# Kernel tuning notes

Hardware: AMD Instinct MI355X
Metric: run time of the kernel (lower is better)

## Reference

```python
import jax, jax.numpy as jnp
import numpy as np

B, T, C, NH, L, V = 2, 1024, 768, 12, 4, 50304
HS = C // NH  # 64


def _norm(x):
    # torch: (x - x.mean(-1)) / x.std(-1) with unbiased std (ddof=1)
    mu = jnp.mean(x, axis=-1, keepdims=True)
    sd = jnp.std(x, axis=-1, ddof=1, keepdims=True)
    return (x - mu) / sd


def setup_inputs() -> dict:
    key = jax.random.key(0)
    ks = jax.random.split(key, 8)
    idx = jax.random.randint(ks[0], (B, T), 0, V)
    wte = jax.random.normal(ks[1], (V, C), jnp.float32) * 0.02
    wpe = jax.random.normal(ks[2], (1024, C), jnp.float32) * 0.02
    c_attn_w = jax.random.normal(ks[3], (L, 3 * C, C), jnp.float32) * 0.02
    c_proj_w = jax.random.normal(ks[4], (L, C, C), jnp.float32) * 0.02
    w_decay = jax.random.uniform(ks[5], (L, C), jnp.float32)          # decay in [0,1)
    eta = jax.random.uniform(ks[6], (L, C), jnp.float32) * 0.01       # small, like 1/block_size init
    lm_head_w = jax.random.normal(ks[7], (V, C), jnp.float32) * 0.02
    return dict(idx=idx, wte=wte, wpe=wpe, c_attn_w=c_attn_w, c_proj_w=c_proj_w,
                w_decay=w_decay, eta=eta, lm_head_w=lm_head_w)


def _rwkv7_block(x, Wqkv, Wproj, wd, et):
    Bx, Tx, Cx = x.shape
    qkv = (x @ Wqkv.T).reshape(Bx, Tx, 3, NH, HS)
    qkv = _norm(qkv)
    # [T, B, nh, hs] each
    q = jnp.transpose(qkv[:, :, 0], (1, 0, 2, 3))
    k = jnp.transpose(qkv[:, :, 1], (1, 0, 2, 3))
    v = jnp.transpose(qkv[:, :, 2], (1, 0, 2, 3))
    q = jax.lax.erf(q)
    k = jax.lax.erf(k)
    wv = wd.reshape(NH, HS)   # decay per (head, channel i)
    ev = et.reshape(NH, HS)
    a = -k
    b = k * ev
    k_ = k * ev
    v_ = v

    def step(state, inp):
        q_t, a_t, b_t, k_t, v_t = inp
        # state: [B, nh, hs(i), hs(k)]
        sab = jnp.einsum('bhik,bhk,bhj->bhij', state, a_t, b_t)
        state = state * wv[None, :, :, None] + sab + jnp.einsum('bhj,bhi->bhij', k_t, v_t)
        out = jnp.einsum('bhj,bhij->bhi', q_t, state)
        return state, out

    state0 = jnp.zeros((Bx, NH, HS, HS), x.dtype)
    _, vt = jax.lax.scan(step, state0, (q, a, b, k_, v_))  # vt: [T, B, nh, hs]
    y = jnp.transpose(vt, (1, 0, 2, 3)).reshape(Bx, Tx, Cx) @ Wproj.T
    return x + y


def reference(idx, wte, wpe, c_attn_w, c_proj_w, w_decay, eta, lm_head_w):
    t = idx.shape[1]
    x = wte[idx] + wpe[:t][None]
    for l in range(L):
        x = _rwkv7_block(x, c_attn_w[l], c_proj_w[l], w_decay[l], eta[l])
    x = _norm(x)
    # targets=None path: logits for last position only
    logits = x[:, -1:, :] @ lm_head_w.T  # [B, 1, V]
    return logits
```

## Files before the change

kernel.cpp:

```cpp
#include <hip/hip_runtime.h>
#include <hip/hip_bf16.h>
#include <cmath>

using bf16   = __bf16;
using bf16x8 = __attribute__((ext_vector_type(8))) __bf16;
using bf16x4 = __attribute__((ext_vector_type(4))) __bf16;
using f32x4  = __attribute__((ext_vector_type(4))) float;
using u32x4  = __attribute__((ext_vector_type(4))) unsigned int;

__global__ __launch_bounds__(256) void cast4_kernel(const float* __restrict__ src,
                                                    bf16* __restrict__ dst, int n4) {
  int i = blockIdx.x * 256 + threadIdx.x;
  int stride = gridDim.x * 256;
  for (; i < n4; i += stride) {
    f32x4 v = ((const f32x4*)src)[i];
    bf16x4 o;
    o[0] = (bf16)v[0]; o[1] = (bf16)v[1]; o[2] = (bf16)v[2]; o[3] = (bf16)v[3];
    ((bf16x4*)dst)[i] = o;
  }
}

__global__ __launch_bounds__(256) void emb_kernel(const int* __restrict__ idx,
                                                  const float* __restrict__ wte,
                                                  const float* __restrict__ wpe,
                                                  float* __restrict__ xf,
                                                  bf16* __restrict__ xb) {
  int bt = blockIdx.x;
  int t = bt & 1023;
  int tok = idx[bt];
  const float* wr = wte + (long)tok * 768;
  const float* pr = wpe + (long)t * 768;
  for (int c = threadIdx.x; c < 768; c += 256) {
    float v = wr[c] + pr[c];
    xf[(long)bt * 768 + c] = v;
    xb[(long)bt * 768 + c] = (bf16)v;
  }
}

template <int PROJ>
__global__ __launch_bounds__(256) void gemm_kernel(const bf16* __restrict__ A,
                                                   const bf16* __restrict__ W,
                                                   float* __restrict__ out,
                                                   float* __restrict__ xf,
                                                   bf16* __restrict__ xb,
                                                   int N, int K) {
  __shared__ char ldsA[128 * 128];
  __shared__ char ldsB[128 * 128];
  const int tid = threadIdx.x;
  const int l = tid & 63, wid = tid >> 6;
  const int lr = l & 15, g = l >> 4;
  const int m0 = blockIdx.y * 128, n0 = blockIdx.x * 128;
  const int wm = wid >> 1, wn = wid & 1;

  f32x4 acc[4][4];
#pragma unroll
  for (int i = 0; i < 4; ++i)
#pragma unroll
    for (int j = 0; j < 4; ++j) acc[i][j] = {0.f, 0.f, 0.f, 0.f};

  for (int k0 = 0; k0 < K; k0 += 32) {
    __syncthreads();
#pragma unroll
    for (int it = 0; it < 2; ++it) {
      int slot = tid + it * 256;
      int row = slot >> 2, q = slot & 3;
      u32x4 da = *(const u32x4*)(A + (long)(m0 + row) * K + k0 + q * 8);
      *(u32x4*)(ldsA + row * 128 + ((q * 16) ^ ((row & 7) << 4))) = da;
      u32x4 db = *(const u32x4*)(W + (long)(n0 + row) * K + k0 + q * 8);
      *(u32x4*)(ldsB + row * 128 + ((q * 16) ^ ((row & 7) << 4))) = db;
    }
    __syncthreads();
    bf16x8 af[4], bfr[4];
#pragma unroll
    for (int it = 0; it < 4; ++it) {
      int row = wm * 64 + it * 16 + lr;
      af[it] = *(const bf16x8*)(ldsA + row * 128 + ((16 * g) ^ ((row & 7) << 4)));
    }
#pragma unroll
    for (int jt = 0; jt < 4; ++jt) {
      int row = wn * 64 + jt * 16 + lr;
      bfr[jt] = *(const bf16x8*)(ldsB + row * 128 + ((16 * g) ^ ((row & 7) << 4)));
    }
#pragma unroll
    for (int it = 0; it < 4; ++it)
#pragma unroll
      for (int jt = 0; jt < 4; ++jt)
        acc[it][jt] = __builtin_amdgcn_mfma_f32_16x16x32_bf16(af[it], bfr[jt], acc[it][jt], 0, 0, 0);
  }

#pragma unroll
  for (int it = 0; it < 4; ++it) {
#pragma unroll
    for (int jt = 0; jt < 4; ++jt) {
      int col = n0 + wn * 64 + jt * 16 + lr;
#pragma unroll
      for (int r = 0; r < 4; ++r) {
        int row = m0 + wm * 64 + it * 16 + g * 4 + r;
        if constexpr (PROJ) {
          long o = (long)row * 768 + col;
          float v = acc[it][jt][r] + xf[o];
          xf[o] = v;
          xb[o] = (bf16)v;
        } else {
          out[(long)row * N + col] = acc[it][jt][r];
        }
      }
    }
  }
}

__global__ __launch_bounds__(256) void normgram_kernel(const float* __restrict__ qkv,
                                                       const float* __restrict__ eta_l,
                                                       bf16* __restrict__ qG,
                                                       bf16* __restrict__ aG,
                                                       float* __restrict__ vG,
                                                       float* __restrict__ GaG,
                                                       bf16* __restrict__ GqG,
                                                       bf16* __restrict__ bTG) {
  const int bh = blockIdx.x >> 6, ch = blockIdx.x & 63;
  const int b = bh / 12, h = bh - b * 12;
  const int tid = threadIdx.x;
  __shared__ float raw[48][68];
  __shared__ float as[16][68], bs[16][68], qs[16][68];

  const long qbase = ((long)(b * 1024 + ch * 16)) * 2304 + h * 64;
#pragma unroll
  for (int i = 0; i < 3; ++i) {
    int slot = tid + i * 256;
    int c4 = slot & 15, sgrp = slot >> 4;
    int t = sgrp / 3, s = sgrp - 3 * t;
    f32x4 d = *(const f32x4*)(qkv + qbase + (long)t * 2304 + s * 768 + c4 * 4);
    *(f32x4*)(&raw[sgrp][c4 * 4]) = d;
  }
  __syncthreads();

  const int l = tid & 63, w = tid >> 6;
  const float ev = eta_l[h * 64 + l];
#pragma unroll
  for (int j = 0; j < 12; ++j) {
    int sgrp = w * 12 + j;
    int t = sgrp / 3, s = sgrp - 3 * t;
    float x = raw[sgrp][l];
    float mu = x;
#pragma unroll
    for (int o = 32; o; o >>= 1) mu += __shfl_xor(mu, o);
    mu *= (1.f / 64.f);
    float d = x - mu;
    float v2 = d * d;
#pragma unroll
    for (int o = 32; o; o >>= 1) v2 += __shfl_xor(v2, o);
    float sd = sqrtf(v2 * (1.f / 63.f));
    float gn = d / sd;
    long base = ((long)bh * 1024 + ch * 16 + t) * 64 + l;
    if (s == 0) {
      float qv = erff(gn);
      qs[t][l] = qv;
      qG[base] = (bf16)qv;
    } else if (s == 1) {
      float kh = erff(gn);
      as[t][l] = -kh;
      bs[t][l] = kh * ev;
      aG[base] = (bf16)(-kh);
    } else {
      vG[base] = gn;
    }
  }
  __syncthreads();

  const int t = tid & 15, u = tid >> 4;
  float dba = 0.f, dbq = 0.f;
#pragma unroll 4
  for (int d = 0; d < 64; ++d) {
    float bv = bs[u][d];
    dba += bv * as[t][d];
    dbq += bv * qs[t][d];
  }
  long g2 = (long)bh * 64 + ch;
  GaG[g2 * 256 + u * 16 + t] = (u < t) ? dba : 0.f;
  GqG[g2 * 512 + t * 32 + u] = (u <= t) ? (bf16)dbq : (bf16)0.f;
  GqG[g2 * 512 + t * 32 + 16 + u] = (bf16)0.f;
  int jj = tid >> 2, uq = tid & 3;
  bf16x8 pkv;
#pragma unroll
  for (int uu = 0; uu < 8; ++uu) pkv[uu] = (uq < 2) ? (bf16)bs[uq * 8 + uu][jj] : (bf16)0.f;
  *(bf16x8*)(bTG + g2 * 2048 + jj * 32 + uq * 8) = pkv;
}

__global__ __launch_bounds__(256) void scan_kernel(const float* __restrict__ wdl,
                                                   const bf16* __restrict__ aG,
                                                   const bf16* __restrict__ qG,
                                                   const float* __restrict__ vG,
                                                   const float* __restrict__ GaG,
                                                   const bf16* __restrict__ GqG,
                                                   const bf16* __restrict__ bTG,
                                                   bf16* __restrict__ yG) {
  const int bh = blockIdx.x;
  const int b = bh / 12, h = bh - b * 12;
  const int tid = threadIdx.x;
  const int l = tid & 63, wid = tid >> 6;
  const int lr = l & 15, g = l >> 4;

  __shared__ char sA[2][2][16 * 128];
  __shared__ char sQ[2][2][16 * 128];
  __shared__ char sB[2][2][64 * 64];
  __shared__ char sG[2][2][16 * 64];
  __shared__ float sGa[2][2][16][16];
  __shared__ float sV[2][2][16][64];
  __shared__ char sS[64 * 128];
  __shared__ float sM[16][68];

  const float* wrow = wdl + h * 64;
  const int irow = wid * 16 + lr;
  const float w_rec = fmaxf(wrow[irow], 0.004f);
  const float winv_rec = 1.0f / w_rec;

  float wc[4], w15c[4], l2wc[4];
#pragma unroll
  for (int r = 0; r < 4; ++r) {
    int row = wid * 16 + g * 4 + r;
    float w = fmaxf(wrow[row], 0.004f);
    wc[r] = w;
    l2wc[r] = log2f(w);
    w15c[r] = exp2f(15.0f * l2wc[r]);
  }

  f32x4 Sf[4];
#pragma unroll
  for (int j = 0; j < 4; ++j) Sf[j] = {0.f, 0.f, 0.f, 0.f};

  const long hTD = (long)bh * 1024 * 64;

  u32x4 rAQ[2], rB[2], rGG[2];
  f32x4 rV[2];

  auto LOAD2 = [&](int c0) {
#pragma unroll
    for (int k = 0; k < 2; ++k) {
      const int c = c0 + k;
      const long tb = hTD + (long)c * 16 * 64;
      const long g2 = (long)bh * 64 + c;
      if (tid < 128) {
        rAQ[k] = *(const u32x4*)(aG + tb + (tid >> 3) * 64 + (tid & 7) * 8);
      } else {
        rAQ[k] = *(const u32x4*)(qG + tb + ((tid - 128) >> 3) * 64 + ((tid - 128) & 7) * 8);
      }
      rB[k] = *(const u32x4*)(bTG + g2 * 2048 + (tid >> 2) * 32 + (tid & 3) * 8);
      if (tid < 64) {
        rGG[k] = *(const u32x4*)(GqG + g2 * 512 + (tid >> 2) * 32 + (tid & 3) * 8);
      } else if (tid < 128) {
        rGG[k] = *(const u32x4*)(GaG + g2 * 256 + ((tid - 64) >> 2) * 16 + ((tid - 64) & 3) * 4);
      }
      rV[k] = *(const f32x4*)(vG + tb + (tid >> 4) * 64 + (tid & 15) * 4);
    }
  };

  auto STORE2 = [&](int nb) {
#pragma unroll
    for (int k = 0; k < 2; ++k) {
      if (tid < 128) {
        int t = tid >> 3, q = tid & 7;
        *(u32x4*)(sA[nb][k] + t * 128 + ((q * 16) ^ ((t & 7) << 4))) = rAQ[k];
      } else {
        int t = (tid - 128) >> 3, q = (tid - 128) & 7;
        *(u32x4*)(sQ[nb][k] + t * 128 + ((q * 16) ^ ((t & 7) << 4))) = rAQ[k];
      }
      {
        int j = tid >> 2, q = tid & 3;
        *(u32x4*)(sB[nb][k] + j * 64 + ((q * 16) ^ ((j & 3) << 4))) = rB[k];
      }
      if (tid < 64) {
        int t = tid >> 2, q = tid & 3;
        *(u32x4*)(sG[nb][k] + t * 64 + ((q * 16) ^ ((t & 3) << 4))) = rGG[k];
      } else if (tid < 128) {
        int u = (tid - 64) >> 2, q = (tid - 64) & 3;
        *(u32x4*)(&sGa[nb][k][u][q * 4]) = rGG[k];
      }
      {
        int t = tid >> 4, i4 = tid & 15;
        *(f32x4*)(&sV[nb][k][t][i4 * 4]) = rV[k];
      }
    }
  };

  auto COMPUTE = [&](int cur, int cip, int ch) {
    const char* pA = sA[cur][cip];
    const char* pQ = sQ[cur][cip];
    const char* pB = sB[cur][cip];
    const char* pG = sG[cur][cip];
    const float* pGa = &sGa[cur][cip][0][0];
    const float* pV = &sV[cur][cip][0][0] + irow;
    const float* pM = &sM[0][0] + irow;

    asm volatile("s_waitcnt lgkmcnt(0)" ::: "memory");
    __builtin_amdgcn_sched_barrier(0);

    f32x4 mf = {0.f, 0.f, 0.f, 0.f}, mqf = {0.f, 0.f, 0.f, 0.f};
#pragma unroll
    for (int s = 0; s < 2; ++s) {
      bf16x8 af = *(const bf16x8*)(sS + irow * 128 + ((64 * s + 16 * g) ^ ((irow & 7) << 4)));
      bf16x8 ba = *(const bf16x8*)(pA + lr * 128 + ((64 * s + 16 * g) ^ ((lr & 7) << 4)));
      bf16x8 bq = *(const bf16x8*)(pQ + lr * 128 + ((64 * s + 16 * g) ^ ((lr & 7) << 4)));
      mf = __builtin_amdgcn_mfma_f32_16x16x32_bf16(af, ba, mf, 0, 0, 0);
      mqf = __builtin_amdgcn_mfma_f32_16x16x32_bf16(af, bq, mqf, 0, 0, 0);
    }
#pragma unroll
    for (int r = 0; r < 4; ++r) sM[lr][wid * 16 + g * 4 + r] = mf[r];
    asm volatile("s_waitcnt lgkmcnt(0)" ::: "memory");
    __builtin_amdgcn_sched_barrier(0);

    f32x4 acc4[4];
#pragma unroll
    for (int t = 0; t < 4; ++t) acc4[t] = {0.f, 0.f, 0.f, 0.f};
    bf16x8 zfrag;
#pragma unroll
    for (int i = 0; i < 8; ++i) zfrag[i] = (bf16)0.0f;
    float wp = 1.f, wpm1 = 0.f, wiv = 1.f;
#pragma unroll
    for (int u = 0; u < 16; ++u) {
      float muv = pM[u * 68];
      float vu = pV[u * 64];
      float c = wp * muv + wpm1 * acc4[u >> 2][u & 3];
      float zt = wiv * (c + vu);
      zfrag[u & 7] = (g == (u >> 3)) ? (bf16)zt : zfrag[u & 7];
      f32x4 ztv = {zt, zt, zt, zt};
#pragma unroll
      for (int q = 0; q < 4; ++q) {
        f32x4 ga = *(const f32x4*)(pGa + u * 16 + q * 4);
        acc4[q] = __builtin_elementwise_fma(ga, ztv, acc4[q]);
      }
      wpm1 = wp;
      wp *= w_rec;
      wiv *= winv_rec;
    }

#pragma unroll
    for (int jt = 0; jt < 4; ++jt) {
      int jrow = jt * 16 + lr;
      bf16x8 bb = *(const bf16x8*)(pB + jrow * 64 + ((16 * g) ^ ((jrow & 3) << 4)));
      f32x4 cs;
#pragma unroll
      for (int r = 0; r < 4; ++r) cs[r] = Sf[jt][r] * wc[r];
      f32x4 ns = __builtin_amdgcn_mfma_f32_16x16x32_bf16(zfrag, bb, cs, 0, 0, 0);
#pragma unroll
      for (int r = 0; r < 4; ++r) Sf[jt][r] = ns[r] * w15c[r];
    }

#pragma unroll
    for (int jt = 0; jt < 4; ++jt) {
#pragma unroll
      for (int r = 0; r < 4; ++r) {
        int row = wid * 16 + g * 4 + r;
        int d = jt * 16 + lr;
        *(bf16*)(sS + row * 128 + ((d * 2) ^ ((row & 7) << 4))) = (bf16)Sf[jt][r];
      }
    }

    {
      bf16x8 gq = *(const bf16x8*)(pG + lr * 64 + ((16 * g) ^ ((lr & 3) << 4)));
      f32x4 cy;
#pragma unroll
      for (int r = 0; r < 4; ++r) cy[r] = mqf[r] * wc[r];
      f32x4 yp = __builtin_amdgcn_mfma_f32_16x16x32_bf16(zfrag, gq, cy, 0, 0, 0);
      bf16x4 yo;
#pragma unroll
      for (int r = 0; r < 4; ++r) yo[r] = (bf16)(yp[r] * exp2f((float)lr * l2wc[r]));
      long yoff = ((long)b * 1024 + ch * 16 + lr) * 768 + h * 64 + wid * 16 + g * 4;
      *(bf16x4*)(yG + yoff) = yo;
    }
  };

  LOAD2(0);
  STORE2(0);
#pragma unroll
  for (int jt = 0; jt < 4; ++jt) {
#pragma unroll
    for (int r = 0; r < 4; ++r) {
      int row = wid * 16 + g * 4 + r;
      int d = jt * 16 + lr;
      *(bf16*)(sS + row * 128 + ((d * 2) ^ ((row & 7) << 4))) = (bf16)0.0f;
    }
  }
  __syncthreads();

  for (int gp = 0; gp < 32; ++gp) {
    const int cur = gp & 1;
    if (gp < 31) LOAD2(2 * gp + 2);
    COMPUTE(cur, 0, 2 * gp);
    COMPUTE(cur, 1, 2 * gp + 1);
    if (gp < 31) STORE2(cur ^ 1);
    __syncthreads();
  }
}

__global__ __launch_bounds__(256) void finalnorm_kernel(const float* __restrict__ xf,
                                                        float* __restrict__ xn) {
  __shared__ float red[4];
  int tid = threadIdx.x;
  for (int b = 0; b < 2; ++b) {
    const float* xr = xf + ((long)b * 1024 + 1023) * 768;
    float s = 0.f;
    for (int c = tid; c < 768; c += 256) s += xr[c];
#pragma unroll
    for (int o = 32; o; o >>= 1) s += __shfl_xor(s, o);
    if ((tid & 63) == 0) red[tid >> 6] = s;
    __syncthreads();
    float mu = (red[0] + red[1] + red[2] + red[3]) * (1.f / 768.f);
    __syncthreads();
    float s2 = 0.f;
    for (int c = tid; c < 768; c += 256) {
      float d = xr[c] - mu;
      s2 += d * d;
    }
#pragma unroll
    for (int o = 32; o; o >>= 1) s2 += __shfl_xor(s2, o);
    if ((tid & 63) == 0) red[tid >> 6] = s2;
    __syncthreads();
    float sd = sqrtf((red[0] + red[1] + red[2] + red[3]) * (1.f / 767.f));
    for (int c = tid; c < 768; c += 256) xn[b * 768 + c] = (xr[c] - mu) / sd;
    __syncthreads();
  }
}

__global__ __launch_bounds__(256) void lmhead_kernel(const float* __restrict__ W,
                                                     const float* __restrict__ xn,
                                                     float* __restrict__ out) {
  int l = threadIdx.x & 63, wid = threadIdx.x >> 6;
  int v0 = blockIdx.x * 64 + wid * 16;
  f32x4 x0[3], x1[3];
#pragma unroll
  for (int i = 0; i < 3; ++i) {
    x0[i] = *(const f32x4*)(xn + l * 4 + i * 256);
    x1[i] = *(const f32x4*)(xn + 768 + l * 4 + i * 256);
  }
  for (int vi = 0; vi < 16; ++vi) {
    const float* wr = W + (long)(v0 + vi) * 768;
    float pa = 0.f, pb = 0.f;
#pragma unroll
    for (int i = 0; i < 3; ++i) {
      f32x4 wv = *(const f32x4*)(wr + l * 4 + i * 256);
#pragma unroll
      for (int r = 0; r < 4; ++r) {
        pa += wv[r] * x0[i][r];
        pb += wv[r] * x1[i][r];
      }
    }
#pragma unroll
    for (int o = 32; o; o >>= 1) {
      pa += __shfl_xor(pa, o);
      pb += __shfl_xor(pb, o);
    }
    if (l == 0) {
      out[v0 + vi] = pa;
      out[50304 + v0 + vi] = pb;
    }
  }
}

extern "C" void kernel_launch(void* const* d_in, const int* in_sizes, int n_in,
                              void* d_out, int out_size, void* d_ws, size_t ws_size,
                              hipStream_t stream) {
  (void)in_sizes; (void)n_in; (void)out_size; (void)ws_size;
  const int*   idx      = (const int*)d_in[0];
  const float* wte      = (const float*)d_in[1];
  const float* wpe      = (const float*)d_in[2];
  const float* c_attn_w = (const float*)d_in[3];
  const float* c_proj_w = (const float*)d_in[4];
  const float* w_decay  = (const float*)d_in[5];
  const float* eta      = (const float*)d_in[6];
  const float* lm_head  = (const float*)d_in[7];
  float* out = (float*)d_out;

  char* ws = (char*)d_ws;
  size_t off = 0;
  auto alloc = [&](size_t bytes) -> char* {
    char* p = ws + off;
    off = (off + bytes + 255) & ~(size_t)255;
    return p;
  };
  float* xf   = (float*)alloc(2L * 1024 * 768 * 4);
  bf16*  xb   = (bf16*)alloc(2L * 1024 * 768 * 2);
  float* qkv  = (float*)alloc(2L * 1024 * 2304 * 4);
  bf16*  qGp  = (bf16*)alloc(24L * 1024 * 64 * 2);
  bf16*  aGp  = (bf16*)alloc(24L * 1024 * 64 * 2);
  float* vGp  = (float*)alloc(24L * 1024 * 64 * 4);
  float* GaGp = (float*)alloc(24L * 64 * 256 * 4);
  bf16*  GqGp = (bf16*)alloc(24L * 64 * 512 * 2);
  bf16*  bTGp = (bf16*)alloc(24L * 64 * 2048 * 2);
  bf16*  yGp  = (bf16*)alloc(2L * 1024 * 768 * 2);
  bf16*  WqB  = (bf16*)alloc(4L * 2304 * 768 * 2);
  bf16*  WpB  = (bf16*)alloc(4L * 768 * 768 * 2);
  float* xn   = (float*)alloc(2L * 768 * 4);

  cast4_kernel<<<dim3(2048), dim3(256), 0, stream>>>(c_attn_w, WqB, 4 * 2304 * 768 / 4);
  cast4_kernel<<<dim3(1024), dim3(256), 0, stream>>>(c_proj_w, WpB, 4 * 768 * 768 / 4);
  emb_kernel<<<dim3(2048), dim3(256), 0, stream>>>(idx, wte, wpe, xf, xb);

  for (int l = 0; l < 4; ++l) {
    gemm_kernel<0><<<dim3(18, 16), dim3(256), 0, stream>>>(
        xb, WqB + (long)l * 2304 * 768, qkv, nullptr, nullptr, 2304, 768);
    normgram_kernel<<<dim3(1536), dim3(256), 0, stream>>>(
        qkv, eta + l * 768, qGp, aGp, vGp, GaGp, GqGp, bTGp);
    scan_kernel<<<dim3(24), dim3(256), 0, stream>>>(
        w_decay + l * 768, aGp, qGp, vGp, GaGp, GqGp, bTGp, yGp);
    gemm_kernel<1><<<dim3(6, 16), dim3(256), 0, stream>>>(
        yGp, WpB + (long)l * 768 * 768, nullptr, xf, xb, 768, 768);
  }

  finalnorm_kernel<<<dim3(1), dim3(256), 0, stream>>>(xf, xn);
  lmhead_kernel<<<dim3(786), dim3(256), 0, stream>>>(lm_head, xn, out);
}
```

Baseline: 797.9 us.

## Split scan per head into four single-wave blocks over state row slices

The scan kernel now launches 96 single-wavefront blocks instead of 24 four-wave blocks. Each block owns 16 of the 64 state rows of one (batch, head) and processes one chunk per iteration. Because the rows of the state recurrence are independent, no cross-wave barrier is needed, so __syncthreads is dropped and the block relies on wave-local LDS ordering. The aim is to spread the serial scan across more CUs and remove block-level sync, at the cost of each block redundantly loading the shared A/Q/B/G chunk data.

```diff
diff --git a/kernel.cpp b/kernel.cpp
--- a/kernel.cpp
+++ b/kernel.cpp
@@ -151,18 +151,18 @@
     for (int o = 32; o; o >>= 1) v2 += __shfl_xor(v2, o);
     float sd = sqrtf(v2 * (1.f / 63.f));
     float gn = d / sd;
-    long base = ((long)bh * 1024 + ch * 16 + t) * 64 + l;
+    long rowb = ((long)bh * 1024 + ch * 16 + t) * 64;
     if (s == 0) {
       float qv = erff(gn);
       qs[t][l] = qv;
-      qG[base] = (bf16)qv;
+      qG[rowb + l] = (bf16)qv;
     } else if (s == 1) {
       float kh = erff(gn);
       as[t][l] = -kh;
       bs[t][l] = kh * ev;
-      aG[base] = (bf16)(-kh);
+      aG[rowb + l] = (bf16)(-kh);
     } else {
-      vG[base] = gn;
+      vG[rowb + l] = gn;
     }
   }
   __syncthreads();
@@ -186,39 +186,38 @@
   *(bf16x8*)(bTG + g2 * 2048 + jj * 32 + uq * 8) = pkv;
 }
 
-__global__ __launch_bounds__(256) void scan_kernel(const float* __restrict__ wdl,
-                                                   const bf16* __restrict__ aG,
-                                                   const bf16* __restrict__ qG,
-                                                   const float* __restrict__ vG,
-                                                   const float* __restrict__ GaG,
-                                                   const bf16* __restrict__ GqG,
-                                                   const bf16* __restrict__ bTG,
-                                                   bf16* __restrict__ yG) {
-  const int bh = blockIdx.x;
+__global__ __launch_bounds__(64) void scan_kernel(const float* __restrict__ wdl,
+                                                  const bf16* __restrict__ aG,
+                                                  const bf16* __restrict__ qG,
+                                                  const float* __restrict__ vG,
+                                                  const float* __restrict__ GaG,
+                                                  const bf16* __restrict__ GqG,
+                                                  const bf16* __restrict__ bTG,
+                                                  bf16* __restrict__ yG) {
+  const int bid = blockIdx.x;
+  const int bh = bid % 24, qi = bid / 24;
   const int b = bh / 12, h = bh - b * 12;
-  const int tid = threadIdx.x;
-  const int l = tid & 63, wid = tid >> 6;
-  const int lr = l & 15, g = l >> 4;
-
-  __shared__ char sA[2][2][16 * 128];
-  __shared__ char sQ[2][2][16 * 128];
-  __shared__ char sB[2][2][64 * 64];
-  __shared__ char sG[2][2][16 * 64];
-  __shared__ float sGa[2][2][16][16];
-  __shared__ float sV[2][2][16][64];
-  __shared__ char sS[64 * 128];
-  __shared__ float sM[16][68];
+  const int i0 = qi * 16;
+  const int l = threadIdx.x;
+  const int g = l >> 4, lr = l & 15;
+
+  __shared__ char  sA[2][16 * 128];
+  __shared__ char  sQ[2][16 * 128];
+  __shared__ char  sB[2][64 * 64];
+  __shared__ char  sG[2][16 * 64];
+  __shared__ float sGa[2][16][16];
+  __shared__ float sV[2][16][16];
+  __shared__ char  sS[16 * 128];
+  __shared__ float sM[16][17];
 
   const float* wrow = wdl + h * 64;
-  const int irow = wid * 16 + lr;
-  const float w_rec = fmaxf(wrow[irow], 0.004f);
-  const float winv_rec = 1.0f / w_rec;
+  const float w_rec = fmaxf(wrow[i0 + lr], 0.004f);
+  const float winv = 1.0f / w_rec;
 
   float wc[4], w15c[4], l2wc[4];
 #pragma unroll
   for (int r = 0; r < 4; ++r) {
-    int row = wid * 16 + g * 4 + r;
-    float w = fmaxf(wrow[row], 0.004f);
+    float w = fmaxf(wrow[i0 + g * 4 + r], 0.004f);
     wc[r] = w;
     l2wc[r] = log2f(w);
     w15c[r] = exp2f(15.0f * l2wc[r]);
@@ -228,83 +227,74 @@
 #pragma unroll
   for (int j = 0; j < 4; ++j) Sf[j] = {0.f, 0.f, 0.f, 0.f};
 
-  const long hTD = (long)bh * 1024 * 64;
-
-  u32x4 rAQ[2], rB[2], rGG[2];
-  f32x4 rV[2];
-
-  auto LOAD2 = [&](int c0) {
-#pragma unroll
-    for (int k = 0; k < 2; ++k) {
-      const int c = c0 + k;
-      const long tb = hTD + (long)c * 16 * 64;
-      const long g2 = (long)bh * 64 + c;
-      if (tid < 128) {
-        rAQ[k] = *(const u32x4*)(aG + tb + (tid >> 3) * 64 + (tid & 7) * 8);
-      } else {
-        rAQ[k] = *(const u32x4*)(qG + tb + ((tid - 128) >> 3) * 64 + ((tid - 128) & 7) * 8);
-      }
-      rB[k] = *(const u32x4*)(bTG + g2 * 2048 + (tid >> 2) * 32 + (tid & 3) * 8);
-      if (tid < 64) {
-        rGG[k] = *(const u32x4*)(GqG + g2 * 512 + (tid >> 2) * 32 + (tid & 3) * 8);
-      } else if (tid < 128) {
-        rGG[k] = *(const u32x4*)(GaG + g2 * 256 + ((tid - 64) >> 2) * 16 + ((tid - 64) & 3) * 4);
-      }
-      rV[k] = *(const f32x4*)(vG + tb + (tid >> 4) * 64 + (tid & 15) * 4);
-    }
+  const long hTD = (long)bh * 65536;
+  const long gB = (long)bh * 64;
+  const int tr = l >> 2, tq = l & 3;
+
+  u32x4 rA0, rA1, rQ0, rQ1, rB[4], rGq;
+  f32x4 rGa, rV;
+
+  auto LOAD = [&](int c) {
+    const long tb = hTD + (long)c * 1024;
+    const bf16* ap = aG + tb + tr * 64 + tq * 16;
+    rA0 = *(const u32x4*)(ap);
+    rA1 = *(const u32x4*)(ap + 8);
+    const bf16* qp = qG + tb + tr * 64 + tq * 16;
+    rQ0 = *(const u32x4*)(qp);
+    rQ1 = *(const u32x4*)(qp + 8);
+    const bf16* bp = bTG + (gB + c) * 2048 + l * 32;
+#pragma unroll
+    for (int k = 0; k < 4; ++k) rB[k] = *(const u32x4*)(bp + k * 8);
+    rGq = *(const u32x4*)(GqG + (gB + c) * 512 + tr * 32 + tq * 8);
+    rGa = *(const f32x4*)(GaG + (gB + c) * 256 + l * 4);
+    rV = *(const f32x4*)(vG + tb + tr * 64 + i0 + tq * 4);
   };
 
-  auto STORE2 = [&](int nb) {
-#pragma unroll
-    for (int k = 0; k < 2; ++k) {
-      if (tid < 128) {
-        int t = tid >> 3, q = tid & 7;
-        *(u32x4*)(sA[nb][k] + t * 128 + ((q * 16) ^ ((t & 7) << 4))) = rAQ[k];
-      } else {
-        int t = (tid - 128) >> 3, q = (tid - 128) & 7;
-        *(u32x4*)(sQ[nb][k] + t * 128 + ((q * 16) ^ ((t & 7) << 4))) = rAQ[k];
-      }
-      {
-        int j = tid >> 2, q = tid & 3;
-        *(u32x4*)(sB[nb][k] + j * 64 + ((q * 16) ^ ((j & 3) << 4))) = rB[k];
-      }
-      if (tid < 64) {
-        int t = tid >> 2, q = tid & 3;
-        *(u32x4*)(sG[nb][k] + t * 64 + ((q * 16) ^ ((t & 3) << 4))) = rGG[k];
-      } else if (tid < 128) {
-        int u = (tid - 64) >> 2, q = (tid - 64) & 3;
-        *(u32x4*)(&sGa[nb][k][u][q * 4]) = rGG[k];
-      }
-      {
-        int t = tid >> 4, i4 = tid & 15;
-        *(f32x4*)(&sV[nb][k][t][i4 * 4]) = rV[k];
-      }
-    }
+  auto STORE = [&](int nb) {
+    const int swzr = (tr & 7) << 4;
+    *(u32x4*)(sA[nb] + tr * 128 + ((tq * 32) ^ swzr)) = rA0;
+    *(u32x4*)(sA[nb] + tr * 128 + ((tq * 32 + 16) ^ swzr)) = rA1;
+    *(u32x4*)(sQ[nb] + tr * 128 + ((tq * 32) ^ swzr)) = rQ0;
+    *(u32x4*)(sQ[nb] + tr * 128 + ((tq * 32 + 16) ^ swzr)) = rQ1;
+#pragma unroll
+    for (int k = 0; k < 4; ++k)
+      *(u32x4*)(sB[nb] + l * 64 + ((k * 16) ^ ((l & 3) << 4))) = rB[k];
+    *(u32x4*)(sG[nb] + tr * 64 + ((tq * 16) ^ ((tr & 3) << 4))) = rGq;
+    *(f32x4*)(&sGa[nb][tr][tq * 4]) = rGa;
+    *(f32x4*)(&sV[nb][tr][tq * 4]) = rV;
   };
 
-  auto COMPUTE = [&](int cur, int cip, int ch) {
-    const char* pA = sA[cur][cip];
-    const char* pQ = sQ[cur][cip];
-    const char* pB = sB[cur][cip];
-    const char* pG = sG[cur][cip];
-    const float* pGa = &sGa[cur][cip][0][0];
-    const float* pV = &sV[cur][cip][0][0] + irow;
-    const float* pM = &sM[0][0] + irow;
-
+  LOAD(0);
+  STORE(0);
+#pragma unroll
+  for (int jt = 0; jt < 4; ++jt) {
+#pragma unroll
+    for (int r = 0; r < 4; ++r) {
+      int row = g * 4 + r;
+      int d = jt * 16 + lr;
+      *(bf16*)(sS + row * 128 + ((d * 2) ^ ((row & 7) << 4))) = (bf16)0.0f;
+    }
+  }
+
+  int cur = 0;
+  for (int c = 0; c < 64; ++c) {
     asm volatile("s_waitcnt lgkmcnt(0)" ::: "memory");
     __builtin_amdgcn_sched_barrier(0);
 
+    if (c < 63) LOAD(c + 1);
+
+    const int swz7 = (lr & 7) << 4, swz3 = (lr & 3) << 4;
     f32x4 mf = {0.f, 0.f, 0.f, 0.f}, mqf = {0.f, 0.f, 0.f, 0.f};
 #pragma unroll
     for (int s = 0; s < 2; ++s) {
-      bf16x8 af = *(const bf16x8*)(sS + irow * 128 + ((64 * s + 16 * g) ^ ((irow & 7) << 4)));
-      bf16x8 ba = *(const bf16x8*)(pA + lr * 128 + ((64 * s + 16 * g) ^ ((lr & 7) << 4)));
-      bf16x8 bq = *(const bf16x8*)(pQ + lr * 128 + ((64 * s + 16 * g) ^ ((lr & 7) << 4)));
+      bf16x8 af = *(const bf16x8*)(sS + lr * 128 + ((64 * s + 16 * g) ^ swz7));
+      bf16x8 ba = *(const bf16x8*)(sA[cur] + lr * 128 + ((64 * s + 16 * g) ^ swz7));
+      bf16x8 bq = *(const bf16x8*)(sQ[cur] + lr * 128 + ((64 * s + 16 * g) ^ swz7));
       mf = __builtin_amdgcn_mfma_f32_16x16x32_bf16(af, ba, mf, 0, 0, 0);
       mqf = __builtin_amdgcn_mfma_f32_16x16x32_bf16(af, bq, mqf, 0, 0, 0);
     }
 #pragma unroll
-    for (int r = 0; r < 4; ++r) sM[lr][wid * 16 + g * 4 + r] = mf[r];
+    for (int r = 0; r < 4; ++r) sM[lr][g * 4 + r] = mf[r];
     asm volatile("s_waitcnt lgkmcnt(0)" ::: "memory");
     __builtin_amdgcn_sched_barrier(0);
 
@@ -317,26 +307,28 @@
     float wp = 1.f, wpm1 = 0.f, wiv = 1.f;
 #pragma unroll
     for (int u = 0; u < 16; ++u) {
-      float muv = pM[u * 68];
-      float vu = pV[u * 64];
-      float c = wp * muv + wpm1 * acc4[u >> 2][u & 3];
-      float zt = wiv * (c + vu);
+      float muv = sM[u][lr];
+      float vu = sV[cur][u][lr];
+      float cc = wp * muv + wpm1 * acc4[u >> 2][u & 3];
+      float zt = wiv * (cc + vu);
       zfrag[u & 7] = (g == (u >> 3)) ? (bf16)zt : zfrag[u & 7];
       f32x4 ztv = {zt, zt, zt, zt};
 #pragma unroll
-      for (int q = 0; q < 4; ++q) {
-        f32x4 ga = *(const f32x4*)(pGa + u * 16 + q * 4);
-        acc4[q] = __builtin_elementwise_fma(ga, ztv, acc4[q]);
+      for (int qq = 0; qq < 4; ++qq) {
+        f32x4 ga = *(const f32x4*)(&sGa[cur][u][qq * 4]);
+        acc4[qq] = __builtin_elementwise_fma(ga, ztv, acc4[qq]);
       }
       wpm1 = wp;
       wp *= w_rec;
-      wiv *= winv_rec;
-    }
+      wiv *= winv;
+    }
+
+    if (c < 63) STORE(cur ^ 1);
 
 #pragma unroll
     for (int jt = 0; jt < 4; ++jt) {
       int jrow = jt * 16 + lr;
-      bf16x8 bb = *(const bf16x8*)(pB + jrow * 64 + ((16 * g) ^ ((jrow & 3) << 4)));
+      bf16x8 bb = *(const bf16x8*)(sB[cur] + jrow * 64 + ((16 * g) ^ ((jrow & 3) << 4)));
       f32x4 cs;
 #pragma unroll
       for (int r = 0; r < 4; ++r) cs[r] = Sf[jt][r] * wc[r];
@@ -349,14 +341,14 @@
     for (int jt = 0; jt < 4; ++jt) {
 #pragma unroll
       for (int r = 0; r < 4; ++r) {
-        int row = wid * 16 + g * 4 + r;
+        int row = g * 4 + r;
         int d = jt * 16 + lr;
         *(bf16*)(sS + row * 128 + ((d * 2) ^ ((row & 7) << 4))) = (bf16)Sf[jt][r];
       }
     }
 
     {
-      bf16x8 gq = *(const bf16x8*)(pG + lr * 64 + ((16 * g) ^ ((lr & 3) << 4)));
+      bf16x8 gq = *(const bf16x8*)(sG[cur] + lr * 64 + ((16 * g) ^ swz3));
       f32x4 cy;
 #pragma unroll
       for (int r = 0; r < 4; ++r) cy[r] = mqf[r] * wc[r];
@@ -364,31 +356,11 @@
       bf16x4 yo;
 #pragma unroll
       for (int r = 0; r < 4; ++r) yo[r] = (bf16)(yp[r] * exp2f((float)lr * l2wc[r]));
-      long yoff = ((long)b * 1024 + ch * 16 + lr) * 768 + h * 64 + wid * 16 + g * 4;
+      long yoff = ((long)b * 1024 + c * 16 + lr) * 768 + h * 64 + i0 + g * 4;
       *(bf16x4*)(yG + yoff) = yo;
     }
-  };
-
-  LOAD2(0);
-  STORE2(0);
-#pragma unroll
-  for (int jt = 0; jt < 4; ++jt) {
-#pragma unroll
-    for (int r = 0; r < 4; ++r) {
-      int row = wid * 16 + g * 4 + r;
-      int d = jt * 16 + lr;
-      *(bf16*)(sS + row * 128 + ((d * 2) ^ ((row & 7) << 4))) = (bf16)0.0f;
-    }
-  }
-  __syncthreads();
-
-  for (int gp = 0; gp < 32; ++gp) {
-    const int cur = gp & 1;
-    if (gp < 31) LOAD2(2 * gp + 2);
-    COMPUTE(cur, 0, 2 * gp);
-    COMPUTE(cur, 1, 2 * gp + 1);
-    if (gp < 31) STORE2(cur ^ 1);
-    __syncthreads();
+
+    cur ^= 1;
   }
 }
 
@@ -500,7 +472,7 @@
         xb, WqB + (long)l * 2304 * 768, qkv, nullptr, nullptr, 2304, 768);
     normgram_kernel<<<dim3(1536), dim3(256), 0, stream>>>(
         qkv, eta + l * 768, qGp, aGp, vGp, GaGp, GqGp, bTGp);
-    scan_kernel<<<dim3(24), dim3(256), 0, stream>>>(
+    scan_kernel<<<dim3(96), dim3(64), 0, stream>>>(
         w_decay + l * 768, aGp, qGp, vGp, GaGp, GqGp, bTGp, yGp);
     gemm_kernel<1><<<dim3(6, 16), dim3(256), 0, stream>>>(
         yGp, WpB + (long)l * 768 * 768, nullptr, xf, xb, 768, 768);
```

After: 921.0 us. +15.4%, slower.

## Fuse head norm and erf into QKV GEMM epilogue, merge prologue and final-norm kernels

Applied to the files above, without the earlier changes.

The QKV GEMM epilogue now does the per-head normalization, erf and eta scaling directly from the accumulators. It uses 16-lane shuffles across each 64-column head tile, which removes the fp32 qkv round trip through global memory. The former normgram kernel becomes a gram kernel that reads the bf16 q/a/b tensors. The weight casts and embedding are merged into one prologue launch, and the final norm is recomputed inside every lm_head block instead of running as a separate single-block kernel. In exchange, every lm_head block redundantly recomputes the norm, and the gram inputs are now rounded to bf16 where they used to be fp32.

```diff
diff --git a/kernel.cpp b/kernel.cpp
--- a/kernel.cpp
+++ b/kernel.cpp
@@ -8,42 +8,50 @@
 using f32x4  = __attribute__((ext_vector_type(4))) float;
 using u32x4  = __attribute__((ext_vector_type(4))) unsigned int;
 
-__global__ __launch_bounds__(256) void cast4_kernel(const float* __restrict__ src,
-                                                    bf16* __restrict__ dst, int n4) {
-  int i = blockIdx.x * 256 + threadIdx.x;
-  int stride = gridDim.x * 256;
-  for (; i < n4; i += stride) {
-    f32x4 v = ((const f32x4*)src)[i];
+__global__ __launch_bounds__(256) void prologue_kernel(const int* __restrict__ idx,
+                                                       const float* __restrict__ wte,
+                                                       const float* __restrict__ wpe,
+                                                       const float* __restrict__ c_attn_w,
+                                                       const float* __restrict__ c_proj_w,
+                                                       float* __restrict__ xf,
+                                                       bf16* __restrict__ xb,
+                                                       bf16* __restrict__ WqB,
+                                                       bf16* __restrict__ WpB) {
+  const int bid = blockIdx.x, tid = threadIdx.x;
+  if (bid < 2048) {
+    int t = bid & 1023;
+    int tok = idx[bid];
+    const float* wr = wte + (long)tok * 768;
+    const float* pr = wpe + (long)t * 768;
+    for (int c = tid; c < 768; c += 256) {
+      float v = wr[c] + pr[c];
+      xf[(long)bid * 768 + c] = v;
+      xb[(long)bid * 768 + c] = (bf16)v;
+    }
+  }
+  const int n4a = 4 * 2304 * 768 / 4;
+  for (int i = bid * 256 + tid; i < n4a; i += 4096 * 256) {
+    f32x4 v = ((const f32x4*)c_attn_w)[i];
     bf16x4 o;
     o[0] = (bf16)v[0]; o[1] = (bf16)v[1]; o[2] = (bf16)v[2]; o[3] = (bf16)v[3];
-    ((bf16x4*)dst)[i] = o;
-  }
-}
-
-__global__ __launch_bounds__(256) void emb_kernel(const int* __restrict__ idx,
-                                                  const float* __restrict__ wte,
-                                                  const float* __restrict__ wpe,
-                                                  float* __restrict__ xf,
-                                                  bf16* __restrict__ xb) {
-  int bt = blockIdx.x;
-  int t = bt & 1023;
-  int tok = idx[bt];
-  const float* wr = wte + (long)tok * 768;
-  const float* pr = wpe + (long)t * 768;
-  for (int c = threadIdx.x; c < 768; c += 256) {
-    float v = wr[c] + pr[c];
-    xf[(long)bt * 768 + c] = v;
-    xb[(long)bt * 768 + c] = (bf16)v;
-  }
-}
-
-template <int PROJ>
-__global__ __launch_bounds__(256) void gemm_kernel(const bf16* __restrict__ A,
-                                                   const bf16* __restrict__ W,
-                                                   float* __restrict__ out,
-                                                   float* __restrict__ xf,
-                                                   bf16* __restrict__ xb,
-                                                   int N, int K) {
+    ((bf16x4*)WqB)[i] = o;
+  }
+  const int n4p = 4 * 768 * 768 / 4;
+  for (int i = bid * 256 + tid; i < n4p; i += 4096 * 256) {
+    f32x4 v = ((const f32x4*)c_proj_w)[i];
+    bf16x4 o;
+    o[0] = (bf16)v[0]; o[1] = (bf16)v[1]; o[2] = (bf16)v[2]; o[3] = (bf16)v[3];
+    ((bf16x4*)WpB)[i] = o;
+  }
+}
+
+__global__ __launch_bounds__(256) void gemmqkv_kernel(const bf16* __restrict__ A,
+                                                      const bf16* __restrict__ W,
+                                                      const float* __restrict__ eta_l,
+                                                      bf16* __restrict__ qG,
+                                                      bf16* __restrict__ aG,
+                                                      bf16* __restrict__ bG,
+                                                      float* __restrict__ vG) {
   __shared__ char ldsA[128 * 128];
   __shared__ char ldsB[128 * 128];
   const int tid = threadIdx.x;
@@ -51,6 +59,7 @@
   const int lr = l & 15, g = l >> 4;
   const int m0 = blockIdx.y * 128, n0 = blockIdx.x * 128;
   const int wm = wid >> 1, wn = wid & 1;
+  const int K = 768;
 
   f32x4 acc[4][4];
 #pragma unroll
@@ -88,6 +97,105 @@
         acc[it][jt] = __builtin_amdgcn_mfma_f32_16x16x32_bf16(af[it], bfr[jt], acc[it][jt], 0, 0, 0);
   }
 
+  const int gi = blockIdx.x * 2 + wn;
+  const int s = gi / 12, h = gi - s * 12;
+  float evc[4];
+#pragma unroll
+  for (int jt = 0; jt < 4; ++jt) evc[jt] = eta_l[h * 64 + jt * 16 + lr];
+
+#pragma unroll
+  for (int it = 0; it < 4; ++it) {
+#pragma unroll
+    for (int r = 0; r < 4; ++r) {
+      int row = m0 + wm * 64 + it * 16 + g * 4 + r;
+      int b = row >> 10, t = row & 1023;
+      float x0 = acc[it][0][r], x1 = acc[it][1][r];
+      float x2 = acc[it][2][r], x3 = acc[it][3][r];
+      float sum = (x0 + x1) + (x2 + x3);
+#pragma unroll
+      for (int o = 8; o; o >>= 1) sum += __shfl_xor(sum, o);
+      float mu = sum * (1.f / 64.f);
+      float d0 = x0 - mu, d1 = x1 - mu, d2 = x2 - mu, d3 = x3 - mu;
+      float v2 = (d0 * d0 + d1 * d1) + (d2 * d2 + d3 * d3);
+#pragma unroll
+      for (int o = 8; o; o >>= 1) v2 += __shfl_xor(v2, o);
+      float sd = sqrtf(v2 * (1.f / 63.f));
+      float gn0 = d0 / sd, gn1 = d1 / sd, gn2 = d2 / sd, gn3 = d3 / sd;
+      long base = ((long)(b * 12 + h) * 1024 + t) * 64 + lr;
+      if (s == 0) {
+        qG[base]      = (bf16)erff(gn0);
+        qG[base + 16] = (bf16)erff(gn1);
+        qG[base + 32] = (bf16)erff(gn2);
+        qG[base + 48] = (bf16)erff(gn3);
+      } else if (s == 1) {
+        float k0 = erff(gn0), k1 = erff(gn1), k2 = erff(gn2), k3 = erff(gn3);
+        aG[base]      = (bf16)(-k0);
+        aG[base + 16] = (bf16)(-k1);
+        aG[base + 32] = (bf16)(-k2);
+        aG[base + 48] = (bf16)(-k3);
+        bG[base]      = (bf16)(k0 * evc[0]);
+        bG[base + 16] = (bf16)(k1 * evc[1]);
+        bG[base + 32] = (bf16)(k2 * evc[2]);
+        bG[base + 48] = (bf16)(k3 * evc[3]);
+      } else {
+        vG[base]      = gn0;
+        vG[base + 16] = gn1;
+        vG[base + 32] = gn2;
+        vG[base + 48] = gn3;
+      }
+    }
+  }
+}
+
+__global__ __launch_bounds__(256) void gemmproj_kernel(const bf16* __restrict__ A,
+                                                       const bf16* __restrict__ W,
+                                                       float* __restrict__ xf,
+                                                       bf16* __restrict__ xb) {
+  __shared__ char ldsA[128 * 128];
+  __shared__ char ldsB[128 * 128];
+  const int tid = threadIdx.x;
+  const int l = tid & 63, wid = tid >> 6;
+  const int lr = l & 15, g = l >> 4;
+  const int m0 = blockIdx.y * 128, n0 = blockIdx.x * 128;
+  const int wm = wid >> 1, wn = wid & 1;
+  const int K = 768;
+
+  f32x4 acc[4][4];
+#pragma unroll
+  for (int i = 0; i < 4; ++i)
+#pragma unroll
+    for (int j = 0; j < 4; ++j) acc[i][j] = {0.f, 0.f, 0.f, 0.f};
+
+  for (int k0 = 0; k0 < K; k0 += 32) {
+    __syncthreads();
+#pragma unroll
+    for (int it = 0; it < 2; ++it) {
+      int slot = tid + it * 256;
+      int row = slot >> 2, q = slot & 3;
+      u32x4 da = *(const u32x4*)(A + (long)(m0 + row) * K + k0 + q * 8);
+      *(u32x4*)(ldsA + row * 128 + ((q * 16) ^ ((row & 7) << 4))) = da;
+      u32x4 db = *(const u32x4*)(W + (long)(n0 + row) * K + k0 + q * 8);
+      *(u32x4*)(ldsB + row * 128 + ((q * 16) ^ ((row & 7) << 4))) = db;
+    }
+    __syncthreads();
+    bf16x8 af[4], bfr[4];
+#pragma unroll
+    for (int it = 0; it < 4; ++it) {
+      int row = wm * 64 + it * 16 + lr;
+      af[it] = *(const bf16x8*)(ldsA + row * 128 + ((16 * g) ^ ((row & 7) << 4)));
+    }
+#pragma unroll
+    for (int jt = 0; jt < 4; ++jt) {
+      int row = wn * 64 + jt * 16 + lr;
+      bfr[jt] = *(const bf16x8*)(ldsB + row * 128 + ((16 * g) ^ ((row & 7) << 4)));
+    }
+#pragma unroll
+    for (int it = 0; it < 4; ++it)
+#pragma unroll
+      for (int jt = 0; jt < 4; ++jt)
+        acc[it][jt] = __builtin_amdgcn_mfma_f32_16x16x32_bf16(af[it], bfr[jt], acc[it][jt], 0, 0, 0);
+  }
+
 #pragma unroll
   for (int it = 0; it < 4; ++it) {
 #pragma unroll
@@ -96,78 +204,32 @@
 #pragma unroll
       for (int r = 0; r < 4; ++r) {
         int row = m0 + wm * 64 + it * 16 + g * 4 + r;
-        if constexpr (PROJ) {
-          long o = (long)row * 768 + col;
-          float v = acc[it][jt][r] + xf[o];
-          xf[o] = v;
-          xb[o] = (bf16)v;
-        } else {
-          out[(long)row * N + col] = acc[it][jt][r];
-        }
-      }
-    }
-  }
-}
-
-__global__ __launch_bounds__(256) void normgram_kernel(const float* __restrict__ qkv,
-                                                       const float* __restrict__ eta_l,
-                                                       bf16* __restrict__ qG,
-                                                       bf16* __restrict__ aG,
-                                                       float* __restrict__ vG,
-                                                       float* __restrict__ GaG,
-                                                       bf16* __restrict__ GqG,
-                                                       bf16* __restrict__ bTG) {
+        long o = (long)row * 768 + col;
+        float v = acc[it][jt][r] + xf[o];
+        xf[o] = v;
+        xb[o] = (bf16)v;
+      }
+    }
+  }
+}
+
+__global__ __launch_bounds__(256) void gram_kernel(const bf16* __restrict__ aG,
+                                                   const bf16* __restrict__ bG,
+                                                   const bf16* __restrict__ qG,
+                                                   float* __restrict__ GaG,
+                                                   bf16* __restrict__ GqG,
+                                                   bf16* __restrict__ bTG) {
   const int bh = blockIdx.x >> 6, ch = blockIdx.x & 63;
-  const int b = bh / 12, h = bh - b * 12;
-  const int tid = threadIdx.x;
-  __shared__ float raw[48][68];
   __shared__ float as[16][68], bs[16][68], qs[16][68];
-
-  const long qbase = ((long)(b * 1024 + ch * 16)) * 2304 + h * 64;
-#pragma unroll
-  for (int i = 0; i < 3; ++i) {
-    int slot = tid + i * 256;
-    int c4 = slot & 15, sgrp = slot >> 4;
-    int t = sgrp / 3, s = sgrp - 3 * t;
-    f32x4 d = *(const f32x4*)(qkv + qbase + (long)t * 2304 + s * 768 + c4 * 4);
-    *(f32x4*)(&raw[sgrp][c4 * 4]) = d;
+  const long tb = ((long)bh * 1024 + ch * 16) * 64;
+  for (int i = threadIdx.x; i < 1024; i += 256) {
+    int t = i >> 6, d = i & 63;
+    as[t][d] = (float)aG[tb + i];
+    bs[t][d] = (float)bG[tb + i];
+    qs[t][d] = (float)qG[tb + i];
   }
   __syncthreads();
-
-  const int l = tid & 63, w = tid >> 6;
-  const float ev = eta_l[h * 64 + l];
-#pragma unroll
-  for (int j = 0; j < 12; ++j) {
-    int sgrp = w * 12 + j;
-    int t = sgrp / 3, s = sgrp - 3 * t;
-    float x = raw[sgrp][l];
-    float mu = x;
-#pragma unroll
-    for (int o = 32; o; o >>= 1) mu += __shfl_xor(mu, o);
-    mu *= (1.f / 64.f);
-    float d = x - mu;
-    float v2 = d * d;
-#pragma unroll
-    for (int o = 32; o; o >>= 1) v2 += __shfl_xor(v2, o);
-    float sd = sqrtf(v2 * (1.f / 63.f));
-    float gn = d / sd;
-    long base = ((long)bh * 1024 + ch * 16 + t) * 64 + l;
-    if (s == 0) {
-      float qv = erff(gn);
-      qs[t][l] = qv;
-      qG[base] = (bf16)qv;
-    } else if (s == 1) {
-      float kh = erff(gn);
-      as[t][l] = -kh;
-      bs[t][l] = kh * ev;
-      aG[base] = (bf16)(-kh);
-    } else {
-      vG[base] = gn;
-    }
-  }
-  __syncthreads();
-
-  const int t = tid & 15, u = tid >> 4;
+  const int t = threadIdx.x & 15, u = threadIdx.x >> 4;
   float dba = 0.f, dbq = 0.f;
 #pragma unroll 4
   for (int d = 0; d < 64; ++d) {
@@ -179,7 +241,7 @@
   GaG[g2 * 256 + u * 16 + t] = (u < t) ? dba : 0.f;
   GqG[g2 * 512 + t * 32 + u] = (u <= t) ? (bf16)dbq : (bf16)0.f;
   GqG[g2 * 512 + t * 32 + 16 + u] = (bf16)0.f;
-  int jj = tid >> 2, uq = tid & 3;
+  int jj = threadIdx.x >> 2, uq = threadIdx.x & 3;
   bf16x8 pkv;
 #pragma unroll
   for (int uu = 0; uu < 8; ++uu) pkv[uu] = (uq < 2) ? (bf16)bs[uq * 8 + uu][jj] : (bf16)0.f;
@@ -212,7 +274,7 @@
   const float* wrow = wdl + h * 64;
   const int irow = wid * 16 + lr;
   const float w_rec = fmaxf(wrow[irow], 0.004f);
-  const float winv_rec = 1.0f / w_rec;
+  const float winv = 1.0f / w_rec;
 
   float wc[4], w15c[4], l2wc[4];
 #pragma unroll
@@ -228,7 +290,8 @@
 #pragma unroll
   for (int j = 0; j < 4; ++j) Sf[j] = {0.f, 0.f, 0.f, 0.f};
 
-  const long hTD = (long)bh * 1024 * 64;
+  const long hTD = (long)bh * 65536;
+  const long gB = (long)bh * 64;
 
   u32x4 rAQ[2], rB[2], rGG[2];
   f32x4 rV[2];
@@ -237,18 +300,17 @@
 #pragma unroll
     for (int k = 0; k < 2; ++k) {
       const int c = c0 + k;
-      const long tb = hTD + (long)c * 16 * 64;
-      const long g2 = (long)bh * 64 + c;
+      const long tb = hTD + (long)c * 1024;
       if (tid < 128) {
         rAQ[k] = *(const u32x4*)(aG + tb + (tid >> 3) * 64 + (tid & 7) * 8);
       } else {
         rAQ[k] = *(const u32x4*)(qG + tb + ((tid - 128) >> 3) * 64 + ((tid - 128) & 7) * 8);
       }
-      rB[k] = *(const u32x4*)(bTG + g2 * 2048 + (tid >> 2) * 32 + (tid & 3) * 8);
+      rB[k] = *(const u32x4*)(bTG + (gB + c) * 2048 + (tid >> 2) * 32 + (tid & 3) * 8);
       if (tid < 64) {
-        rGG[k] = *(const u32x4*)(GqG + g2 * 512 + (tid >> 2) * 32 + (tid & 3) * 8);
+        rGG[k] = *(const u32x4*)(GqG + (gB + c) * 512 + (tid >> 2) * 32 + (tid & 3) * 8);
       } else if (tid < 128) {
-        rGG[k] = *(const u32x4*)(GaG + g2 * 256 + ((tid - 64) >> 2) * 16 + ((tid - 64) & 3) * 4);
+        rGG[k] = *(const u32x4*)(GaG + (gB + c) * 256 + ((tid - 64) >> 2) * 16 + ((tid - 64) & 3) * 4);
       }
       rV[k] = *(const f32x4*)(vG + tb + (tid >> 4) * 64 + (tid & 15) * 4);
     }
@@ -319,18 +381,18 @@
     for (int u = 0; u < 16; ++u) {
       float muv = pM[u * 68];
       float vu = pV[u * 64];
-      float c = wp * muv + wpm1 * acc4[u >> 2][u & 3];
-      float zt = wiv * (c + vu);
+      float cc = wp * muv + wpm1 * acc4[u >> 2][u & 3];
+      float zt = wiv * (cc + vu);
       zfrag[u & 7] = (g == (u >> 3)) ? (bf16)zt : zfrag[u & 7];
       f32x4 ztv = {zt, zt, zt, zt};
 #pragma unroll
-      for (int q = 0; q < 4; ++q) {
-        f32x4 ga = *(const f32x4*)(pGa + u * 16 + q * 4);
-        acc4[q] = __builtin_elementwise_fma(ga, ztv, acc4[q]);
+      for (int qq = 0; qq < 4; ++qq) {
+        f32x4 ga = *(const f32x4*)(pGa + u * 16 + qq * 4);
+        acc4[qq] = __builtin_elementwise_fma(ga, ztv, acc4[qq]);
       }
       wpm1 = wp;
       wp *= w_rec;
-      wiv *= winv_rec;
+      wiv *= winv;
     }
 
 #pragma unroll
@@ -392,10 +454,12 @@
   }
 }
 
-__global__ __launch_bounds__(256) void finalnorm_kernel(const float* __restrict__ xf,
-                                                        float* __restrict__ xn) {
+__global__ __launch_bounds__(256) void lmhead_kernel(const float* __restrict__ W,
+                                                     const float* __restrict__ xf,
+                                                     float* __restrict__ out) {
+  __shared__ float xn[2][768];
   __shared__ float red[4];
-  int tid = threadIdx.x;
+  const int tid = threadIdx.x;
   for (int b = 0; b < 2; ++b) {
     const float* xr = xf + ((long)b * 1024 + 1023) * 768;
     float s = 0.f;
@@ -416,21 +480,17 @@
     if ((tid & 63) == 0) red[tid >> 6] = s2;
     __syncthreads();
     float sd = sqrtf((red[0] + red[1] + red[2] + red[3]) * (1.f / 767.f));
-    for (int c = tid; c < 768; c += 256) xn[b * 768 + c] = (xr[c] - mu) / sd;
-    __syncthreads();
-  }
-}
-
-__global__ __launch_bounds__(256) void lmhead_kernel(const float* __restrict__ W,
-                                                     const float* __restrict__ xn,
-                                                     float* __restrict__ out) {
-  int l = threadIdx.x & 63, wid = threadIdx.x >> 6;
+    for (int c = tid; c < 768; c += 256) xn[b][c] = (xr[c] - mu) / sd;
+    __syncthreads();
+  }
+
+  int l = tid & 63, wid = tid >> 6;
   int v0 = blockIdx.x * 64 + wid * 16;
   f32x4 x0[3], x1[3];
 #pragma unroll
   for (int i = 0; i < 3; ++i) {
-    x0[i] = *(const f32x4*)(xn + l * 4 + i * 256);
-    x1[i] = *(const f32x4*)(xn + 768 + l * 4 + i * 256);
+    x0[i] = *(const f32x4*)(&xn[0][l * 4 + i * 256]);
+    x1[i] = *(const f32x4*)(&xn[1][l * 4 + i * 256]);
   }
   for (int vi = 0; vi < 16; ++vi) {
     const float* wr = W + (long)(v0 + vi) * 768;
@@ -479,9 +539,9 @@
   };
   float* xf   = (float*)alloc(2L * 1024 * 768 * 4);
   bf16*  xb   = (bf16*)alloc(2L * 1024 * 768 * 2);
-  float* qkv  = (float*)alloc(2L * 1024 * 2304 * 4);
   bf16*  qGp  = (bf16*)alloc(24L * 1024 * 64 * 2);
   bf16*  aGp  = (bf16*)alloc(24L * 1024 * 64 * 2);
+  bf16*  bGp  = (bf16*)alloc(24L * 1024 * 64 * 2);
   float* vGp  = (float*)alloc(24L * 1024 * 64 * 4);
   float* GaGp = (float*)alloc(24L * 64 * 256 * 4);
   bf16*  GqGp = (bf16*)alloc(24L * 64 * 512 * 2);
@@ -489,23 +549,19 @@
   bf16*  yGp  = (bf16*)alloc(2L * 1024 * 768 * 2);
   bf16*  WqB  = (bf16*)alloc(4L * 2304 * 768 * 2);
   bf16*  WpB  = (bf16*)alloc(4L * 768 * 768 * 2);
-  float* xn   = (float*)alloc(2L * 768 * 4);
-
-  cast4_kernel<<<dim3(2048), dim3(256), 0, stream>>>(c_attn_w, WqB, 4 * 2304 * 768 / 4);
-  cast4_kernel<<<dim3(1024), dim3(256), 0, stream>>>(c_proj_w, WpB, 4 * 768 * 768 / 4);
-  emb_kernel<<<dim3(2048), dim3(256), 0, stream>>>(idx, wte, wpe, xf, xb);
+
+  prologue_kernel<<<dim3(4096), dim3(256), 0, stream>>>(
+      idx, wte, wpe, c_attn_w, c_proj_w, xf, xb, WqB, WpB);
 
   for (int l = 0; l < 4; ++l) {
-    gemm_kernel<0><<<dim3(18, 16), dim3(256), 0, stream>>>(
-        xb, WqB + (long)l * 2304 * 768, qkv, nullptr, nullptr, 2304, 768);
-    normgram_kernel<<<dim3(1536), dim3(256), 0, stream>>>(
-        qkv, eta + l * 768, qGp, aGp, vGp, GaGp, GqGp, bTGp);
+    gemmqkv_kernel<<<dim3(18, 16), dim3(256), 0, stream>>>(
+        xb, WqB + (long)l * 2304 * 768, eta + l * 768, qGp, aGp, bGp, vGp);
+    gram_kernel<<<dim3(1536), dim3(256), 0, stream>>>(aGp, bGp, qGp, GaGp, GqGp, bTGp);
     scan_kernel<<<dim3(24), dim3(256), 0, stream>>>(
         w_decay + l * 768, aGp, qGp, vGp, GaGp, GqGp, bTGp, yGp);
-    gemm_kernel<1><<<dim3(6, 16), dim3(256), 0, stream>>>(
-        yGp, WpB + (long)l * 768 * 768, nullptr, xf, xb, 768, 768);
-  }
-
-  finalnorm_kernel<<<dim3(1), dim3(256), 0, stream>>>(xf, xn);
-  lmhead_kernel<<<dim3(786), dim3(256), 0, stream>>>(lm_head, xn, out);
-}
+    gemmproj_kernel<<<dim3(6, 16), dim3(256), 0, stream>>>(
+        yGp, WpB + (long)l * 768 * 768, xf, xb);
+  }
+
+  lmhead_kernel<<<dim3(786), dim3(256), 0, stream>>>(lm_head, xf, out);
+}
```

Measured after the change: 781.3 us. -2.1%, faster.
